# Performance work log

Measured on AMD Instinct MI355X. Metric: run time of the kernel, lower is better.

The kernel has to match this reference:

```python
import jax, jax.numpy as jnp
import numpy as np

B, S, HLEN, VLEN, HID = 32, 2048, 1024, 1024, 1024


def setup_inputs() -> dict:
    key = jax.random.key(0)
    ks = jax.random.split(key, 6)
    scale_W = 1.0 / np.sqrt(HLEN)
    scale_U = 1.0 / np.sqrt(VLEN)
    scale_w = 1.0 / np.sqrt(HID)
    return {
        "h": jax.random.normal(ks[0], (B, HLEN), dtype=jnp.float32),
        "V": jax.random.normal(ks[1], (B, S, VLEN), dtype=jnp.float32),
        "W_w": jax.random.normal(ks[2], (HID, HLEN), dtype=jnp.float32) * scale_W,
        "W_b": jax.random.normal(ks[3], (HID,), dtype=jnp.float32) * scale_W,
        "U_w": jax.random.normal(ks[4], (HID, VLEN), dtype=jnp.float32) * scale_U,
        "w_w": jax.random.normal(ks[5], (HID,), dtype=jnp.float32) * scale_w,
    }


def reference(h, V, W_w, W_b, U_w, w_w):
    # e = w^T tanh(W h + U V^T + b); beta = softmax(e); out = sum_s beta_s V_s
    h_proj = h @ W_w.T + W_b                      # [B, HID]
    V_proj = jnp.einsum('bsv,dv->bsd', V, U_w)    # [B, S, HID]
    e = jnp.einsum('bsd,d->bs', jnp.tanh(h_proj[:, None, :] + V_proj), w_w)  # [B, S]
    beta = jax.nn.softmax(e, axis=1)              # [B, S]
    return jnp.einsum('bs,bsv->bv', beta, V)      # [B, VLEN]
```

## Files before the change

### kernel.cpp

```cpp
#include <hip/hip_runtime.h>

constexpr int B_   = 32;
constexpr int S_   = 2048;
constexpr int HID_ = 1024;
constexpr int VL_  = 1024;

typedef __attribute__((ext_vector_type(4))) float  f32x4;
typedef __attribute__((ext_vector_type(4))) short  s16x4;
typedef __attribute__((ext_vector_type(8))) short  s16x8;

__device__ __forceinline__ short f2bf(float f) {
    union { float f; unsigned u; } v; v.f = f;
    unsigned r = v.u + 0x7fffu + ((v.u >> 16) & 1u);
    return (short)(r >> 16);
}

__device__ __forceinline__ float bf2f(short s) {
    union { unsigned u; float f; } v;
    v.u = ((unsigned)(unsigned short)s) << 16;
    return v.f;
}

__device__ __forceinline__ float fast_tanh(float x) {
    float e2 = __expf(2.0f * x);
    return 1.0f - 2.0f / (e2 + 1.0f);
}

__device__ __forceinline__ void async_cp16(const void* g, void* l) {
    __builtin_amdgcn_global_load_lds(
        (const __attribute__((address_space(1))) unsigned int*)g,
        (__attribute__((address_space(3))) unsigned int*)l,
        16, 0, 0);
}

__global__ __launch_bounds__(256) void hproj_kernel(const float* __restrict__ h,
                                                    const float* __restrict__ Ww,
                                                    const float* __restrict__ Wb,
                                                    float* __restrict__ hp) {
    int tid = threadIdx.x;
    int wave = tid >> 6, lane = tid & 63;
    int d = blockIdx.x * 4 + wave;
    const float* wr = Ww + (size_t)d * HID_;
    float4 wreg[4];
#pragma unroll
    for (int i = 0; i < 4; i++) wreg[i] = *(const float4*)(wr + i * 256 + lane * 4);
    float bias = Wb[d];
    for (int b = 0; b < B_; b++) {
        const float* hr = h + (size_t)b * HID_;
        float acc = 0.0f;
#pragma unroll
        for (int i = 0; i < 4; i++) {
            float4 x = *(const float4*)(hr + i * 256 + lane * 4);
            acc += wreg[i].x * x.x + wreg[i].y * x.y + wreg[i].z * x.z + wreg[i].w * x.w;
        }
#pragma unroll
        for (int o = 32; o; o >>= 1) acc += __shfl_xor(acc, o);
        if (lane == 0) hp[(size_t)b * HID_ + d] = acc + bias;
    }
}

__global__ __launch_bounds__(256) void cvt_kernel(const float* __restrict__ src,
                                                  short* __restrict__ dst, size_t n4) {
    size_t i = (size_t)blockIdx.x * blockDim.x + threadIdx.x;
    size_t stride = (size_t)gridDim.x * blockDim.x;
    for (; i < n4; i += stride) {
        float4 x = ((const float4*)src)[i];
        s16x4 y;
        y.x = f2bf(x.x); y.y = f2bf(x.y); y.z = f2bf(x.z); y.w = f2bf(x.w);
        ((s16x4*)dst)[i] = y;
    }
}

constexpr int BM_E = 256;
constexpr int BK_E = 64;
constexpr int NT_E = VL_ / BK_E;

__global__ __launch_bounds__(512, 2) void e_kernel_8ph(const short* __restrict__ Vm,
                                                       const short* __restrict__ Um,
                                                       const float* __restrict__ hp,
                                                       const float* __restrict__ ww,
                                                       float* __restrict__ e) {
    __shared__ short Al[2][BM_E][BK_E];
    __shared__ short Bl[2][BM_E][BK_E];

    const int tid  = threadIdx.x;
    const int wave = tid >> 6, lane = tid & 63;
    const int wm = wave >> 2, wn = wave & 3;
    const int col = lane & 15, quad = lane >> 4;
    const int rx  = col & 7;
    const int s0 = blockIdx.x * BM_E;
    const int b  = blockIdx.y;

    const int srow   = lane >> 3;
    const int schunk = (lane & 7) ^ srow;

    const short* gA = Vm + ((size_t)b * S_ + s0 + wave * 8 + srow) * VL_ + schunk * 8;
    const short* gB = Um + (size_t)(wave * 8 + srow) * VL_ + schunk * 8;

    float ep[8][4];
#pragma unroll
    for (int i = 0; i < 8; i++)
#pragma unroll
        for (int j = 0; j < 4; j++) ep[i][j] = 0.0f;

    for (int dt = 0; dt < 4; ++dt) {
        const int d0 = dt * 256;

        f32x4 acc[8][4];
        f32x4 zero = {0.f, 0.f, 0.f, 0.f};
#pragma unroll
        for (int i = 0; i < 8; i++)
#pragma unroll
            for (int j = 0; j < 4; j++) acc[i][j] = zero;

#pragma unroll
        for (int r = 0; r < 4; ++r) {
            async_cp16(gA + (size_t)(r * 64) * VL_, &Al[0][r * 64 + wave * 8][0]);
            async_cp16(gB + ((size_t)(d0 + r * 64)) * VL_, &Bl[0][r * 64 + wave * 8][0]);
        }
        asm volatile("s_waitcnt vmcnt(0)" ::: "memory");
        __builtin_amdgcn_s_barrier();

        for (int t = 0; t < NT_E; ++t) {
            const int c = t & 1;
            s16x8 b8[4][2];
            s16x8 a8[2][2];
#pragma unroll
            for (int p = 0; p < 4; ++p) {
#pragma unroll
                for (int i = 0; i < 2; ++i)
#pragma unroll
                    for (int kk = 0; kk < 2; ++kk)
                        a8[i][kk] = *(const s16x8*)&Al[c][wm * 128 + (2 * p + i) * 16 + col]
                                                        [((((kk << 2) | quad) ^ rx) << 3)];
                if (p == 0) {
#pragma unroll
                    for (int tn = 0; tn < 4; ++tn)
#pragma unroll
                        for (int kk = 0; kk < 2; ++kk)
                            b8[tn][kk] = *(const s16x8*)&Bl[c][wn * 64 + tn * 16 + col]
                                                             [((((kk << 2) | quad) ^ rx) << 3)];
                }
                if (p == 0 && t + 1 < NT_E) {
                    const short* g = gA + (size_t)(t + 1) * BK_E;
#pragma unroll
                    for (int r = 0; r < 4; ++r)
                        async_cp16(g + (size_t)(r * 64) * VL_, &Al[c ^ 1][r * 64 + wave * 8][0]);
                }
                if (p == 1 && t + 1 < NT_E) {
                    const short* g = gB + (size_t)d0 * VL_ + (size_t)(t + 1) * BK_E;
#pragma unroll
                    for (int r = 0; r < 4; ++r)
                        async_cp16(g + (size_t)(r * 64) * VL_, &Bl[c ^ 1][r * 64 + wave * 8][0]);
                }
                __builtin_amdgcn_s_barrier();
                __builtin_amdgcn_s_setprio(1);
#pragma unroll
                for (int kk = 0; kk < 2; ++kk)
#pragma unroll
                    for (int i = 0; i < 2; ++i)
#pragma unroll
                        for (int tn = 0; tn < 4; ++tn)
                            acc[2 * p + i][tn] = __builtin_amdgcn_mfma_f32_16x16x32_bf16(
                                a8[i][kk], b8[tn][kk], acc[2 * p + i][tn], 0, 0, 0);
                __builtin_amdgcn_s_setprio(0);
                if (p == 3)
                    asm volatile("s_waitcnt vmcnt(0)" ::: "memory");
                __builtin_amdgcn_s_barrier();
            }
        }

        float wv[4], hv[4];
#pragma unroll
        for (int tn = 0; tn < 4; ++tn) {
            int d = d0 + wn * 64 + tn * 16 + col;
            wv[tn] = ww[d];
            hv[tn] = hp[(size_t)b * HID_ + d];
        }
#pragma unroll
        for (int tm = 0; tm < 8; ++tm)
#pragma unroll
            for (int reg = 0; reg < 4; ++reg)
#pragma unroll
                for (int tn = 0; tn < 4; ++tn)
                    ep[tm][reg] += wv[tn] * fast_tanh(hv[tn] + acc[tm][tn][reg]);
    }

    float* eb = (float*)&Al[0][0][0];
#pragma unroll
    for (int tm = 0; tm < 8; ++tm)
#pragma unroll
        for (int reg = 0; reg < 4; ++reg) {
            float p = ep[tm][reg];
            p += __shfl_xor(p, 1);
            p += __shfl_xor(p, 2);
            p += __shfl_xor(p, 4);
            p += __shfl_xor(p, 8);
            if (col == 0)
                eb[wn * 256 + wm * 128 + tm * 16 + quad * 4 + reg] = p;
        }
    __syncthreads();
    if (tid < 256)
        e[(size_t)b * S_ + s0 + tid] =
            eb[tid] + eb[256 + tid] + eb[512 + tid] + eb[768 + tid];
}

__global__ __launch_bounds__(256) void e_kernel_f32(const float* __restrict__ Vm,
                                                    const float* __restrict__ Um,
                                                    const float* __restrict__ hp,
                                                    const float* __restrict__ ww,
                                                    float* __restrict__ e) {
    __shared__ short As[128][40];
    __shared__ short Bs[128][40];
    int tid = threadIdx.x;
    int b  = blockIdx.z;
    int d0 = blockIdx.x * 128;
    int s0 = blockIdx.y * 128;
    int wave = tid >> 6, lane = tid & 63;
    int wm = wave >> 1, wn = wave & 1;
    int col = lane & 15, quad = lane >> 4;

    f32x4 zero = {0.f, 0.f, 0.f, 0.f};
    f32x4 acc[4][4];
#pragma unroll
    for (int i = 0; i < 4; i++)
#pragma unroll
        for (int j = 0; j < 4; j++) acc[i][j] = zero;

    const float* Abase = Vm + ((size_t)b * S_ + s0) * (size_t)VL_;
    const float* Bbase = Um + (size_t)d0 * (size_t)VL_;

    for (int k0 = 0; k0 < VL_; k0 += 32) {
        int k4 = tid & 7, rb = tid >> 3;
#pragma unroll
        for (int i = 0; i < 4; i++) {
            int r = rb + 32 * i;
            float4 x = *(const float4*)(Abase + (size_t)r * VL_ + k0 + k4 * 4);
            s16x4 ya; ya.x = f2bf(x.x); ya.y = f2bf(x.y); ya.z = f2bf(x.z); ya.w = f2bf(x.w);
            *(s16x4*)&As[r][k4 * 4] = ya;
            float4 y = *(const float4*)(Bbase + (size_t)r * VL_ + k0 + k4 * 4);
            s16x4 yb; yb.x = f2bf(y.x); yb.y = f2bf(y.y); yb.z = f2bf(y.z); yb.w = f2bf(y.w);
            *(s16x4*)&Bs[r][k4 * 4] = yb;
        }
        __syncthreads();
        s16x8 a8[4], b8[4];
#pragma unroll
        for (int tm = 0; tm < 4; tm++)
            a8[tm] = *(const s16x8*)&As[wm * 64 + tm * 16 + col][quad * 8];
#pragma unroll
        for (int tn = 0; tn < 4; tn++)
            b8[tn] = *(const s16x8*)&Bs[wn * 64 + tn * 16 + col][quad * 8];
#pragma unroll
        for (int tm = 0; tm < 4; tm++)
#pragma unroll
            for (int tn = 0; tn < 4; tn++)
                acc[tm][tn] = __builtin_amdgcn_mfma_f32_16x16x32_bf16(
                    a8[tm], b8[tn], acc[tm][tn], 0, 0, 0);
        __syncthreads();
    }

    float wv[4], hv[4];
#pragma unroll
    for (int tn = 0; tn < 4; tn++) {
        int d = d0 + wn * 64 + tn * 16 + col;
        wv[tn] = ww[d];
        hv[tn] = hp[(size_t)b * HID_ + d];
    }
#pragma unroll
    for (int tm = 0; tm < 4; tm++) {
#pragma unroll
        for (int reg = 0; reg < 4; reg++) {
            float p = 0.0f;
#pragma unroll
            for (int tn = 0; tn < 4; tn++)
                p += wv[tn] * fast_tanh(hv[tn] + acc[tm][tn][reg]);
            p += __shfl_xor(p, 1);
            p += __shfl_xor(p, 2);
            p += __shfl_xor(p, 4);
            p += __shfl_xor(p, 8);
            if (col == 0) {
                int s = s0 + wm * 64 + tm * 16 + quad * 4 + reg;
                atomicAdd(&e[(size_t)b * S_ + s], p);
            }
        }
    }
}

__global__ __launch_bounds__(256) void softmax_kernel(const float* __restrict__ epart,
                                                      float* __restrict__ beta,
                                                      int nparts) {
    int b = blockIdx.x, tid = threadIdx.x;
    const float* r0 = epart + (size_t)b * S_;
    const float* r1 = epart + ((size_t)B_ + b) * S_;
    float v[8];
    float m = -1e30f;
#pragma unroll
    for (int i = 0; i < 8; i++) {
        int idx = tid + i * 256;
        v[i] = r0[idx] + (nparts > 1 ? r1[idx] : 0.0f);
        m = fmaxf(m, v[i]);
    }
#pragma unroll
    for (int o = 32; o; o >>= 1) m = fmaxf(m, __shfl_xor(m, o));
    __shared__ float rm[4], rs[4];
    int wave = tid >> 6, lane = tid & 63;
    if (lane == 0) rm[wave] = m;
    __syncthreads();
    m = fmaxf(fmaxf(rm[0], rm[1]), fmaxf(rm[2], rm[3]));
    float s = 0.0f;
#pragma unroll
    for (int i = 0; i < 8; i++) { v[i] = __expf(v[i] - m); s += v[i]; }
#pragma unroll
    for (int o = 32; o; o >>= 1) s += __shfl_xor(s, o);
    if (lane == 0) rs[wave] = s;
    __syncthreads();
    s = rs[0] + rs[1] + rs[2] + rs[3];
    float inv = 1.0f / s;
#pragma unroll
    for (int i = 0; i < 8; i++) beta[(size_t)b * S_ + tid + i * 256] = v[i] * inv;
}

__global__ __launch_bounds__(256) void out_kernel_bf16(const float* __restrict__ beta,
                                                       const short* __restrict__ Vb16,
                                                       float* __restrict__ opart) {
    int b = blockIdx.x, sc = blockIdx.y;
    int v4 = threadIdx.x;
    const short* Vp = Vb16 + ((size_t)b * S_ + (size_t)sc * 128) * VL_;
    const float* bb = beta + (size_t)b * S_ + (size_t)sc * 128;
    float ax = 0.f, ay = 0.f, az = 0.f, aw = 0.f;
    for (int s = 0; s < 128; s++) {
        float w = bb[s];
        s16x4 x = *(const s16x4*)(Vp + (size_t)s * VL_ + v4 * 4);
        ax += w * bf2f(x.x); ay += w * bf2f(x.y);
        az += w * bf2f(x.z); aw += w * bf2f(x.w);
    }
    float4 r = {ax, ay, az, aw};
    *(float4*)(opart + (((size_t)b * 16 + sc) * VL_) + v4 * 4) = r;
}

__global__ __launch_bounds__(256) void out_reduce_kernel(const float* __restrict__ opart,
                                                         float* __restrict__ out) {
    int b = blockIdx.x, v4 = threadIdx.x;
    float4 a = {0.f, 0.f, 0.f, 0.f};
    const float* base = opart + (size_t)b * 16 * VL_;
#pragma unroll
    for (int sc = 0; sc < 16; sc++) {
        float4 x = *(const float4*)(base + (size_t)sc * VL_ + v4 * 4);
        a.x += x.x; a.y += x.y; a.z += x.z; a.w += x.w;
    }
    *(float4*)(out + (size_t)b * VL_ + v4 * 4) = a;
}

__global__ __launch_bounds__(256) void out_kernel_f32(const float* __restrict__ beta,
                                                      const float* __restrict__ V,
                                                      float* __restrict__ out) {
    int b = blockIdx.x, sc = blockIdx.y;
    int v4 = threadIdx.x;
    const float* Vb = V + ((size_t)b * S_ + (size_t)sc * 128) * VL_;
    const float* bb = beta + (size_t)b * S_ + (size_t)sc * 128;
    float ax = 0.f, ay = 0.f, az = 0.f, aw = 0.f;
    for (int s = 0; s < 128; s++) {
        float w = bb[s];
        float4 x = *(const float4*)(Vb + (size_t)s * VL_ + v4 * 4);
        ax += w * x.x; ay += w * x.y; az += w * x.z; aw += w * x.w;
    }
    float* o = out + (size_t)b * VL_ + v4 * 4;
    atomicAdd(o + 0, ax);
    atomicAdd(o + 1, ay);
    atomicAdd(o + 2, az);
    atomicAdd(o + 3, aw);
}

extern "C" void kernel_launch(void* const* d_in, const int* in_sizes, int n_in,
                              void* d_out, int out_size, void* d_ws, size_t ws_size,
                              hipStream_t stream) {
    const float* h  = (const float*)d_in[0];
    const float* V  = (const float*)d_in[1];
    const float* Ww = (const float*)d_in[2];
    const float* Wb = (const float*)d_in[3];
    const float* Uw = (const float*)d_in[4];
    const float* ww = (const float*)d_in[5];
    float* out = (float*)d_out;

    char* ws = (char*)d_ws;
    float* hp    = (float*)ws;
    float* epart = (float*)(ws + 131072);
    float* beta  = (float*)(ws + 131072 + 524288);
    float* opart = (float*)(ws + 131072 + 524288 + 262144);
    size_t fixed = 131072 + 524288 + 262144 + 2097152;
    short* Vb16 = (short*)(ws + fixed);
    short* Ub16 = Vb16 + (size_t)B_ * S_ * VL_;
    size_t need = fixed + ((size_t)B_ * S_ * VL_ + (size_t)HID_ * VL_) * 2;
    bool bf16path = (ws_size >= need);

    hproj_kernel<<<dim3(HID_ / 4), 256, 0, stream>>>(h, Ww, Wb, hp);

    if (bf16path) {
        cvt_kernel<<<4096, 256, 0, stream>>>(V, Vb16, (size_t)B_ * S_ * VL_ / 4);
        cvt_kernel<<<256, 256, 0, stream>>>(Uw, Ub16, (size_t)HID_ * VL_ / 4);
        e_kernel_8ph<<<dim3(S_ / BM_E, B_), 512, 0, stream>>>(Vb16, Ub16, hp, ww, epart);
        softmax_kernel<<<B_, 256, 0, stream>>>(epart, beta, 1);
        out_kernel_bf16<<<dim3(B_, S_ / 128), 256, 0, stream>>>(beta, Vb16, opart);
        out_reduce_kernel<<<B_, 256, 0, stream>>>(opart, out);
    } else {
        hipMemsetAsync(epart, 0, (size_t)B_ * S_ * 4, stream);
        hipMemsetAsync(out, 0, (size_t)out_size * 4, stream);
        e_kernel_f32<<<dim3(HID_ / 128, S_ / 128, B_), 256, 0, stream>>>(
            V, Uw, hp, ww, epart);
        softmax_kernel<<<B_, 256, 0, stream>>>(epart, beta, 1);
        out_kernel_f32<<<dim3(B_, S_ / 128), 256, 0, stream>>>(beta, V, out);
    }
}
```

Measured before the change: 593.6 us.

## Flatten HID-tile loop into single pipelined K loop with staggered prefetch waits

Merges the outer loop over four 256-wide HID tiles and the inner K loop into one continuous loop of 64 steps. The double-buffered prefetch now runs across tile boundaries, so the pipeline no longer drains and refills at each new HID tile. Prefetch loads are spread evenly over the four phases and waited on with partial vmcnt counts instead of a full drain. The tanh epilogue runs inline every 16 steps, which adds a branch and makes the vmcnt accounting more fragile.

```diff
diff --git a/kernel.cpp b/kernel.cpp
--- a/kernel.cpp
+++ b/kernel.cpp
@@ -73,7 +73,7 @@
 
 constexpr int BM_E = 256;
 constexpr int BK_E = 64;
-constexpr int NT_E = VL_ / BK_E;
+constexpr int NT_ALL = 4 * (VL_ / BK_E);
 
 __global__ __launch_bounds__(512, 2) void e_kernel_8ph(const short* __restrict__ Vm,
                                                        const short* __restrict__ Um,
@@ -94,8 +94,8 @@
     const int srow   = lane >> 3;
     const int schunk = (lane & 7) ^ srow;
 
-    const short* gA = Vm + ((size_t)b * S_ + s0 + wave * 8 + srow) * VL_ + schunk * 8;
-    const short* gB = Um + (size_t)(wave * 8 + srow) * VL_ + schunk * 8;
+    const short* gAb = Vm + ((size_t)b * S_ + s0 + wave * 8 + srow) * VL_ + schunk * 8;
+    const short* gBb = Um + (size_t)(wave * 8 + srow) * VL_ + schunk * 8;
 
     float ep[8][4];
 #pragma unroll
@@ -103,87 +103,105 @@
 #pragma unroll
         for (int j = 0; j < 4; j++) ep[i][j] = 0.0f;
 
-    for (int dt = 0; dt < 4; ++dt) {
-        const int d0 = dt * 256;
-
-        f32x4 acc[8][4];
-        f32x4 zero = {0.f, 0.f, 0.f, 0.f};
-#pragma unroll
-        for (int i = 0; i < 8; i++)
-#pragma unroll
-            for (int j = 0; j < 4; j++) acc[i][j] = zero;
-
-#pragma unroll
-        for (int r = 0; r < 4; ++r) {
-            async_cp16(gA + (size_t)(r * 64) * VL_, &Al[0][r * 64 + wave * 8][0]);
-            async_cp16(gB + ((size_t)(d0 + r * 64)) * VL_, &Bl[0][r * 64 + wave * 8][0]);
-        }
-        asm volatile("s_waitcnt vmcnt(0)" ::: "memory");
-        __builtin_amdgcn_s_barrier();
-
-        for (int t = 0; t < NT_E; ++t) {
-            const int c = t & 1;
-            s16x8 b8[4][2];
+    f32x4 acc[8][4];
+    f32x4 zero = {0.f, 0.f, 0.f, 0.f};
+#pragma unroll
+    for (int i = 0; i < 8; i++)
+#pragma unroll
+        for (int j = 0; j < 4; j++) acc[i][j] = zero;
+
+#pragma unroll
+    for (int r = 0; r < 4; ++r) {
+        async_cp16(gAb + (size_t)(r * 64) * VL_, &Al[0][r * 64 + wave * 8][0]);
+        async_cp16(gBb + (size_t)(r * 64) * VL_, &Bl[0][r * 64 + wave * 8][0]);
+    }
+    asm volatile("s_waitcnt vmcnt(0)" ::: "memory");
+    __builtin_amdgcn_s_barrier();
+
+    for (int T = 0; T < NT_ALL; ++T) {
+        const int c  = T & 1;
+        const bool pf = (T + 1 < NT_ALL);
+        const int ktn = (T + 1) & 15;
+        const size_t dtn = (size_t)((T + 1) >> 4);
+        const short* gAn = gAb + ktn * BK_E;
+        const short* gBn = gBb + (dtn * 256) * VL_ + ktn * BK_E;
+
+        s16x8 b8[4][2];
+#pragma unroll
+        for (int p = 0; p < 4; ++p) {
             s16x8 a8[2][2];
 #pragma unroll
-            for (int p = 0; p < 4; ++p) {
+            for (int i = 0; i < 2; ++i)
+#pragma unroll
+                for (int kk = 0; kk < 2; ++kk)
+                    a8[i][kk] = *(const s16x8*)&Al[c][wm * 128 + (2 * p + i) * 16 + col]
+                                                    [((((kk << 2) | quad) ^ rx) << 3)];
+            if (p == 0) {
+#pragma unroll
+                for (int tn = 0; tn < 4; ++tn)
+#pragma unroll
+                    for (int kk = 0; kk < 2; ++kk)
+                        b8[tn][kk] = *(const s16x8*)&Bl[c][wn * 64 + tn * 16 + col]
+                                                         [((((kk << 2) | quad) ^ rx) << 3)];
+            }
+            if (pf) {
+                if (p == 0) {
+                    async_cp16(gBn,                        &Bl[c ^ 1][wave * 8][0]);
+                    async_cp16(gBn + (size_t)64 * VL_,     &Bl[c ^ 1][64 + wave * 8][0]);
+                } else if (p == 1) {
+                    async_cp16(gBn + (size_t)128 * VL_,    &Bl[c ^ 1][128 + wave * 8][0]);
+                    async_cp16(gBn + (size_t)192 * VL_,    &Bl[c ^ 1][192 + wave * 8][0]);
+                } else if (p == 2) {
+                    async_cp16(gAn,                        &Al[c ^ 1][wave * 8][0]);
+                    async_cp16(gAn + (size_t)128 * VL_,    &Al[c ^ 1][128 + wave * 8][0]);
+                } else {
+                    async_cp16(gAn + (size_t)64 * VL_,     &Al[c ^ 1][64 + wave * 8][0]);
+                    async_cp16(gAn + (size_t)192 * VL_,    &Al[c ^ 1][192 + wave * 8][0]);
+                }
+            }
+            __builtin_amdgcn_s_barrier();
+            __builtin_amdgcn_s_setprio(1);
+#pragma unroll
+            for (int kk = 0; kk < 2; ++kk)
 #pragma unroll
                 for (int i = 0; i < 2; ++i)
 #pragma unroll
-                    for (int kk = 0; kk < 2; ++kk)
-                        a8[i][kk] = *(const s16x8*)&Al[c][wm * 128 + (2 * p + i) * 16 + col]
-                                                        [((((kk << 2) | quad) ^ rx) << 3)];
-                if (p == 0) {
-#pragma unroll
                     for (int tn = 0; tn < 4; ++tn)
-#pragma unroll
-                        for (int kk = 0; kk < 2; ++kk)
-                            b8[tn][kk] = *(const s16x8*)&Bl[c][wn * 64 + tn * 16 + col]
-                                                             [((((kk << 2) | quad) ^ rx) << 3)];
-                }
-                if (p == 0 && t + 1 < NT_E) {
-                    const short* g = gA + (size_t)(t + 1) * BK_E;
-#pragma unroll
-                    for (int r = 0; r < 4; ++r)
-                        async_cp16(g + (size_t)(r * 64) * VL_, &Al[c ^ 1][r * 64 + wave * 8][0]);
-                }
-                if (p == 1 && t + 1 < NT_E) {
-                    const short* g = gB + (size_t)d0 * VL_ + (size_t)(t + 1) * BK_E;
-#pragma unroll
-                    for (int r = 0; r < 4; ++r)
-                        async_cp16(g + (size_t)(r * 64) * VL_, &Bl[c ^ 1][r * 64 + wave * 8][0]);
-                }
-                __builtin_amdgcn_s_barrier();
-                __builtin_amdgcn_s_setprio(1);
-#pragma unroll
-                for (int kk = 0; kk < 2; ++kk)
-#pragma unroll
-                    for (int i = 0; i < 2; ++i)
-#pragma unroll
-                        for (int tn = 0; tn < 4; ++tn)
-                            acc[2 * p + i][tn] = __builtin_amdgcn_mfma_f32_16x16x32_bf16(
-                                a8[i][kk], b8[tn][kk], acc[2 * p + i][tn], 0, 0, 0);
-                __builtin_amdgcn_s_setprio(0);
-                if (p == 3)
+                        acc[2 * p + i][tn] = __builtin_amdgcn_mfma_f32_16x16x32_bf16(
+                            a8[i][kk], b8[tn][kk], acc[2 * p + i][tn], 0, 0, 0);
+            __builtin_amdgcn_s_setprio(0);
+            if (p == 1) {
+                asm volatile("s_waitcnt vmcnt(4)" ::: "memory");
+            } else if (p == 3) {
+                if (T == NT_ALL - 2)
                     asm volatile("s_waitcnt vmcnt(0)" ::: "memory");
-                __builtin_amdgcn_s_barrier();
+                else
+                    asm volatile("s_waitcnt vmcnt(2)" ::: "memory");
             }
-        }
-
-        float wv[4], hv[4];
-#pragma unroll
-        for (int tn = 0; tn < 4; ++tn) {
-            int d = d0 + wn * 64 + tn * 16 + col;
-            wv[tn] = ww[d];
-            hv[tn] = hp[(size_t)b * HID_ + d];
-        }
-#pragma unroll
-        for (int tm = 0; tm < 8; ++tm)
-#pragma unroll
-            for (int reg = 0; reg < 4; ++reg)
-#pragma unroll
-                for (int tn = 0; tn < 4; ++tn)
-                    ep[tm][reg] += wv[tn] * fast_tanh(hv[tn] + acc[tm][tn][reg]);
+            __builtin_amdgcn_s_barrier();
+        }
+
+        if ((T & 15) == 15) {
+            const int d0 = (T >> 4) * 256;
+            float wv[4], hv[4];
+#pragma unroll
+            for (int tn = 0; tn < 4; ++tn) {
+                int d = d0 + wn * 64 + tn * 16 + col;
+                wv[tn] = ww[d];
+                hv[tn] = hp[(size_t)b * HID_ + d];
+            }
+#pragma unroll
+            for (int tm = 0; tm < 8; ++tm)
+#pragma unroll
+                for (int reg = 0; reg < 4; ++reg)
+#pragma unroll
+                    for (int tn = 0; tn < 4; ++tn)
+                        ep[tm][reg] += wv[tn] * fast_tanh(hv[tn] + acc[tm][tn][reg]);
+#pragma unroll
+            for (int i = 0; i < 8; i++)
+#pragma unroll
+                for (int j = 0; j < 4; j++) acc[i][j] = zero;
+        }
     }
 
     float* eb = (float*)&Al[0][0][0];
```

After: 596.6 us. Within noise of the previous version (+0.5%).
